# Optimization experiments

Measured on AMD Instinct MI355X. Metric: run time of the kernel, lower is better.

The kernel has to match this reference:

```python
import jax, jax.numpy as jnp
import numpy as np

N = 8192
IN = 32          # Config.network_in_size
G = 16           # Config.global_size
H1 = 32          # layer1 out
H2 = 16          # lstm vertex out
LSTM_HID = H2 + G      # 48
LSTM_IN = H1 * 3 + G   # 112
L3_IN = H2 * 3 + G     # 64
EPS = 1e-12


def _norm_l1(a):
    # F.normalize(a, p=1, dim=-1): divide by max(L1-norm, eps)
    return a / jnp.maximum(jnp.sum(jnp.abs(a), axis=-1, keepdims=True), EPS)


def _leaky(v):
    return jnp.where(v >= 0, v, 0.01 * v)


def setup_inputs() -> dict:
    key = jax.random.key(0)
    ks = jax.random.split(key, 12)
    s = lambda fan: 1.0 / np.sqrt(fan)
    inp = {
        'adj': jax.random.uniform(ks[0], (N, N), dtype=jnp.float32),
        'x': jax.random.normal(ks[1], (N, IN), dtype=jnp.float32),
        'h': jnp.zeros((N, LSTM_HID), jnp.float32),
        'c': jnp.zeros((N, LSTM_HID), jnp.float32),
        # layer1 GraphLinear(32->32, u->16), input 3*32=96
        'W1': jax.random.uniform(ks[2], (H1, IN * 3), jnp.float32, -s(IN * 3), s(IN * 3)),
        'b1': jnp.zeros((H1,), jnp.float32),
        'uW1': jax.random.uniform(ks[3], (G, IN * 3), jnp.float32, -s(IN * 3), s(IN * 3)),
        'ub1': jnp.zeros((G,), jnp.float32),
        # layer2 LSTM(112 -> 48)
        'Wih': jax.random.uniform(ks[4], (4 * LSTM_HID, LSTM_IN), jnp.float32, -s(LSTM_HID), s(LSTM_HID)),
        'Whh': jax.random.uniform(ks[5], (4 * LSTM_HID, LSTM_HID), jnp.float32, -s(LSTM_HID), s(LSTM_HID)),
        'bih': jnp.zeros((4 * LSTM_HID,), jnp.float32),
        'bhh': jnp.zeros((4 * LSTM_HID,), jnp.float32),
        # layer3 GraphLinear(16->3, in_global=16), input 3*16+16=64
        'W3': jax.random.uniform(ks[6], (3, L3_IN), jnp.float32, -s(L3_IN), s(L3_IN)),
        'b3': jnp.zeros((3,), jnp.float32),
    }
    return inp


def _policy_core(adj, x, h, c, W1, b1, uW1, ub1, Wih, Whh, bih, bhh, W3, b3):
    A = _norm_l1(adj)          # row-normalized adjacency
    AT = _norm_l1(adj.T)       # row-normalized transpose

    # --- layer 1: GraphLinear (no global input) ---
    l1 = jnp.concatenate([A @ x, AT @ x, x], axis=-1)             # [N, 96]
    v1 = _leaky(l1 @ W1.T + b1)                                    # [N, 32]
    u1 = _leaky(jnp.mean(l1, axis=-2) @ uW1.T + ub1)               # [16]

    # --- layer 2: GraphLSTM (seq_len=1, batch=N) ---
    l2 = jnp.concatenate([
        jnp.broadcast_to(u1, (v1.shape[0], G)),
        A @ v1, AT @ v1, v1], axis=-1)                             # [N, 112]
    gates = l2 @ Wih.T + bih + h @ Whh.T + bhh                     # [N, 192]
    i, f, g, o = jnp.split(gates, 4, axis=-1)
    c_out = jax.nn.sigmoid(f) * c + jax.nn.sigmoid(i) * jnp.tanh(g)
    h_out = jax.nn.sigmoid(o) * jnp.tanh(c_out)                    # [N, 48]
    v2 = _leaky(h_out[:, :H2])                                     # [N, 16]
    u2 = _leaky(jnp.mean(h_out[:, H2:], axis=-2))                  # [16]

    # --- layer 3: GraphLinear with global input (no activation) ---
    l3 = jnp.concatenate([
        jnp.broadcast_to(u2, (v2.shape[0], G)),
        A @ v2, AT @ v2, v2], axis=-1)                             # [N, 64]
    x3 = l3 @ W3.T + b3                                            # [N, 3]

    logits = 2.0 * jnp.tanh(x3)
    probs = jax.nn.softmax(logits, axis=-1)
    return probs, logits, h_out, c_out


def reference(adj, x, h, c, W1, b1, uW1, ub1, Wih, Whh, bih, bhh, W3, b3):
    probs, logits, h_out, c_out = _policy_core(
        adj, x, h, c, W1, b1, uW1, ub1, Wih, Whh, bih, bhh, W3, b3)
    # multinomial(probs, 1) == categorical over the same logits
    actions = jax.random.categorical(jax.random.key(42), logits, axis=-1)  # [N]
    return (actions.astype(jnp.float32) - 1.0, h_out, c_out)
```

## Files before the change

### kernel.cpp

```cpp
#include <hip/hip_runtime.h>
#include <stdint.h>
#include <math.h>

#define NROW 8192

constexpr size_t W_FP  = 0;
constexpr size_t W_GP  = W_FP  + (size_t)32*NROW*32;
constexpr size_t W_RSP = W_GP  + (size_t)64*NROW*32;
constexpr size_t W_CSP = W_RSP + (size_t)32*NROW;
constexpr size_t W_RS  = W_CSP + (size_t)64*NROW;
constexpr size_t W_CS  = W_RS  + NROW;
constexpr size_t W_V1  = W_CS  + NROW;
constexpr size_t W_V2  = W_V1  + (size_t)NROW*32;
constexpr size_t W_U1  = W_V2  + (size_t)NROW*16;
constexpr size_t W_MLP = W_U1  + 16;
constexpr size_t W_U2P = W_MLP + (size_t)256*96;

typedef float f32x4 __attribute__((ext_vector_type(4)));
typedef short s16x8 __attribute__((ext_vector_type(8)));

__device__ __forceinline__ float leaky(float v) { return v >= 0.f ? v : 0.01f * v; }
__device__ __forceinline__ float sigf(float v) { return 1.f / (1.f + __expf(-v)); }
__device__ __forceinline__ double leakyd(double v) { return v >= 0. ? v : 0.01 * v; }

__device__ __forceinline__ uint32_t bf16rne(float x) {
  uint32_t b = __float_as_uint(x);
  return (b + 0x7FFFu + ((b >> 16) & 1u)) >> 16;
}
__device__ __forceinline__ float bf2f(short s) {
  return __uint_as_float(((uint32_t)(uint16_t)s) << 16);
}
__device__ __forceinline__ uint32_t packHL(float x) {
  const uint32_t hb = bf16rne(x);
  const float hf = __uint_as_float(hb << 16);
  const uint32_t lb = bf16rne(x - hf);
  return hb | (lb << 16);
}
__device__ __forceinline__ void unpack8(const uint32_t u[8], s16x8& h, s16x8& l) {
  #pragma unroll
  for (int j = 0; j < 8; ++j) { h[j] = (short)(u[j] & 0xffffu); l[j] = (short)(u[j] >> 16); }
}

__device__ __forceinline__ void threefry(uint32_t x0, uint32_t x1, uint32_t& o0, uint32_t& o1) {
  const uint32_t ks0 = 0u, ks1 = 42u;
  const uint32_t ks2 = ks0 ^ ks1 ^ 0x1BD11BDAu;
  uint32_t ks[3] = {ks0, ks1, ks2};
  const int R0[4] = {13, 15, 26, 6};
  const int R1[4] = {17, 29, 16, 24};
  x0 += ks[0]; x1 += ks[1];
  #pragma unroll
  for (int g = 0; g < 5; ++g) {
    const int* R = (g & 1) ? R1 : R0;
    #pragma unroll
    for (int i = 0; i < 4; ++i) {
      x0 += x1;
      x1 = (x1 << R[i]) | (x1 >> (32 - R[i]));
      x1 ^= x0;
    }
    x0 += ks[(g + 1) % 3];
    x1 += ks[(g + 2) % 3] + (uint32_t)(g + 1);
  }
  o0 = x0; o1 = x1;
}

template <int C, bool SUMS>
__global__ __launch_bounds__(256) void k_gemm(const float* __restrict__ adj,
                                              const float* __restrict__ X,
                                              float* __restrict__ Fp,
                                              float* __restrict__ Gp,
                                              float* __restrict__ rsP,
                                              float* __restrict__ csP) {
  constexpr int NT = C / 16;
  __shared__ alignas(16) uint32_t aP[32 * 132];
  __shared__ alignas(16) short X2h[C * 136];
  __shared__ alignas(16) short X2l[C * 136];
  __shared__ alignas(16) short XkH[C * 40];
  __shared__ alignas(16) short XkL[C * 40];
  const int t = threadIdx.x;
  const int iz = blockIdx.x;
  const int kz = blockIdx.y;
  const int I0 = iz * 128;
  const int K0 = kz * 256;
  const int lane = t & 63;
  const int wid = t >> 6;
  const int fm = lane & 15;
  const int fg = lane >> 4;

  if constexpr (C == 32) {
    #pragma unroll
    for (int r = 0; r < 4; ++r) {
      const int i = r * 32 + (t >> 3);
      const int c4 = 4 * (t & 7);
      const float4 v = *(const float4*)&X[(size_t)(I0 + i) * 32 + c4];
      const float vv[4] = {v.x, v.y, v.z, v.w};
      #pragma unroll
      for (int j = 0; j < 4; ++j) {
        const uint32_t p = packHL(vv[j]);
        X2h[(c4 + j) * 136 + i] = (short)(p & 0xffffu);
        X2l[(c4 + j) * 136 + i] = (short)(p >> 16);
      }
    }
  } else {
    if (t < 128) {
      #pragma unroll
      for (int r = 0; r < 4; ++r) {
        const int i = r * 32 + (t >> 2);
        const int c4 = 4 * (t & 3);
        const float4 v = *(const float4*)&X[(size_t)(I0 + i) * 16 + c4];
        const float vv[4] = {v.x, v.y, v.z, v.w};
        #pragma unroll
        for (int j = 0; j < 4; ++j) {
          const uint32_t p = packHL(vv[j]);
          X2h[(c4 + j) * 136 + i] = (short)(p & 0xffffu);
          X2l[(c4 + j) * 136 + i] = (short)(p >> 16);
        }
      }
    }
  }

  f32x4 accF[4][NT];
  #pragma unroll
  for (int mt = 0; mt < 4; ++mt)
    #pragma unroll
    for (int nt = 0; nt < NT; ++nt) accF[mt][nt] = (f32x4){0.f, 0.f, 0.f, 0.f};
  float rs[4] = {0.f, 0.f, 0.f, 0.f};

  const int rb = t >> 3;
  const int k4 = 4 * (t & 7);

  for (int ch = 0; ch < 8; ++ch) {
    const int kb = K0 + ch * 32;
    __syncthreads();
    #pragma unroll
    for (int q = 0; q < 4; ++q) {
      const int i = q * 32 + rb;
      const float4 v = *(const float4*)&adj[(size_t)(I0 + i) * NROW + kb + k4];
      const float vv[4] = {v.x, v.y, v.z, v.w};
      #pragma unroll
      for (int j = 0; j < 4; ++j) aP[(k4 + j) * 132 + i] = packHL(vv[j]);
    }
    if constexpr (C == 32) {
      const int k = t >> 3, c4 = 4 * (t & 7);
      const float4 v = *(const float4*)&X[(size_t)(kb + k) * 32 + c4];
      const float vv[4] = {v.x, v.y, v.z, v.w};
      #pragma unroll
      for (int j = 0; j < 4; ++j) {
        const uint32_t p = packHL(vv[j]);
        XkH[(c4 + j) * 40 + k] = (short)(p & 0xffffu);
        XkL[(c4 + j) * 40 + k] = (short)(p >> 16);
      }
    } else {
      if (t < 128) {
        const int k = t >> 2, c4 = 4 * (t & 3);
        const float4 v = *(const float4*)&X[(size_t)(kb + k) * 16 + c4];
        const float vv[4] = {v.x, v.y, v.z, v.w};
        #pragma unroll
        for (int j = 0; j < 4; ++j) {
          const uint32_t p = packHL(vv[j]);
          XkH[(c4 + j) * 40 + k] = (short)(p & 0xffffu);
          XkL[(c4 + j) * 40 + k] = (short)(p >> 16);
        }
      }
    }
    __syncthreads();
    if (wid < 2) {
      s16x8 bh[NT], bl[NT];
      #pragma unroll
      for (int nt = 0; nt < NT; ++nt) {
        bh[nt] = *(const s16x8*)&XkH[(nt * 16 + fm) * 40 + 8 * fg];
        bl[nt] = *(const s16x8*)&XkL[(nt * 16 + fm) * 40 + 8 * fg];
      }
      #pragma unroll
      for (int mt = 0; mt < 4; ++mt) {
        const int rowl = (wid * 4 + mt) * 16 + fm;
        uint32_t u[8];
        #pragma unroll
        for (int j = 0; j < 8; ++j) u[j] = aP[(8 * fg + j) * 132 + rowl];
        s16x8 ah, al;
        unpack8(u, ah, al);
        if (SUMS) {
          #pragma unroll
          for (int j = 0; j < 8; ++j) rs[mt] += fabsf(bf2f(ah[j]) + bf2f(al[j]));
        }
        #pragma unroll
        for (int nt = 0; nt < NT; ++nt) {
          accF[mt][nt] = __builtin_amdgcn_mfma_f32_16x16x32_bf16(ah, bh[nt], accF[mt][nt], 0, 0, 0);
          accF[mt][nt] = __builtin_amdgcn_mfma_f32_16x16x32_bf16(ah, bl[nt], accF[mt][nt], 0, 0, 0);
          accF[mt][nt] = __builtin_amdgcn_mfma_f32_16x16x32_bf16(al, bh[nt], accF[mt][nt], 0, 0, 0);
        }
      }
    } else {
      const int kt = wid - 2;
      f32x4 accT[NT];
      #pragma unroll
      for (int ct = 0; ct < NT; ++ct) accT[ct] = (f32x4){0.f, 0.f, 0.f, 0.f};
      float cs = 0.f;
      #pragma unroll
      for (int iw = 0; iw < 4; ++iw) {
        const uint32_t* ap = &aP[(kt * 16 + fm) * 132 + iw * 32 + 8 * fg];
        const uint4 ua = *(const uint4*)ap;
        const uint4 ub = *(const uint4*)(ap + 4);
        const uint32_t u[8] = {ua.x, ua.y, ua.z, ua.w, ub.x, ub.y, ub.z, ub.w};
        s16x8 ah, al;
        unpack8(u, ah, al);
        if (SUMS) {
          #pragma unroll
          for (int j = 0; j < 8; ++j) cs += fabsf(bf2f(ah[j]) + bf2f(al[j]));
        }
        #pragma unroll
        for (int ct = 0; ct < NT; ++ct) {
          const s16x8 xh = *(const s16x8*)&X2h[(ct * 16 + fm) * 136 + iw * 32 + 8 * fg];
          const s16x8 xl = *(const s16x8*)&X2l[(ct * 16 + fm) * 136 + iw * 32 + 8 * fg];
          accT[ct] = __builtin_amdgcn_mfma_f32_16x16x32_bf16(ah, xh, accT[ct], 0, 0, 0);
          accT[ct] = __builtin_amdgcn_mfma_f32_16x16x32_bf16(ah, xl, accT[ct], 0, 0, 0);
          accT[ct] = __builtin_amdgcn_mfma_f32_16x16x32_bf16(al, xh, accT[ct], 0, 0, 0);
        }
      }
      #pragma unroll
      for (int ct = 0; ct < NT; ++ct)
        #pragma unroll
        for (int r = 0; r < 4; ++r)
          Gp[((size_t)iz * NROW + kb + kt * 16 + 4 * fg + r) * C + ct * 16 + fm] = accT[ct][r];
      if (SUMS) {
        cs += __shfl_xor(cs, 16, 64);
        cs += __shfl_xor(cs, 32, 64);
        if (lane < 16) csP[(size_t)iz * NROW + kb + kt * 16 + lane] = cs;
      }
    }
  }
  if (wid < 2) {
    #pragma unroll
    for (int mt = 0; mt < 4; ++mt) {
      const int rowb = I0 + (wid * 4 + mt) * 16;
      #pragma unroll
      for (int nt = 0; nt < NT; ++nt)
        #pragma unroll
        for (int r = 0; r < 4; ++r)
          Fp[((size_t)kz * NROW + rowb + 4 * fg + r) * C + nt * 16 + fm] = accF[mt][nt][r];
      if (SUMS) {
        float v = rs[mt];
        v += __shfl_xor(v, 16, 64);
        v += __shfl_xor(v, 32, 64);
        if (lane < 16) rsP[(size_t)kz * NROW + rowb + lane] = v;
      }
    }
  }
}

__global__ __launch_bounds__(256) void k_s1(const float* __restrict__ Fp, const float* __restrict__ rsP,
                                            const float* __restrict__ Gp, const float* __restrict__ csP,
                                            const float* __restrict__ x,  const float* __restrict__ W1,
                                            const float* __restrict__ b1,
                                            float* __restrict__ rowsum, float* __restrict__ colsum,
                                            float* __restrict__ v1, float* __restrict__ mlp) {
  __shared__ float l1L[32 * 100];
  __shared__ float rsL[32], csL[32];
  const int t = threadIdx.x;
  const int n0 = blockIdx.x * 32;
  if (t < 32) {
    double s = 0.;
    for (int p = 0; p < 32; ++p) s += (double)rsP[(size_t)p * NROW + n0 + t];
    s = fmax(s, 1e-12);
    rowsum[n0 + t] = (float)s; rsL[t] = (float)s;
  } else if (t < 64) {
    const int r = t - 32;
    double s = 0.;
    for (int p = 0; p < 64; ++p) s += (double)csP[(size_t)p * NROW + n0 + r];
    s = fmax(s, 1e-12);
    colsum[n0 + r] = (float)s; csL[r] = (float)s;
  }
  __syncthreads();
  {
    const int r = t >> 3, c = (t & 7) * 4;
    const int n = n0 + r;
    double s[4] = {0., 0., 0., 0.};
    for (int p = 0; p < 32; ++p) {
      const float4 v = *(const float4*)&Fp[((size_t)p * NROW + n) * 32 + c];
      s[0] += v.x; s[1] += v.y; s[2] += v.z; s[3] += v.w;
    }
    const double rsv = (double)rsL[r];
    #pragma unroll
    for (int q = 0; q < 4; ++q) l1L[r * 100 + c + q] = (float)(s[q] / rsv);
    double sg[4] = {0., 0., 0., 0.};
    for (int p = 0; p < 64; ++p) {
      const float4 v = *(const float4*)&Gp[((size_t)p * NROW + n) * 32 + c];
      sg[0] += v.x; sg[1] += v.y; sg[2] += v.z; sg[3] += v.w;
    }
    const double csv = (double)csL[r];
    #pragma unroll
    for (int q = 0; q < 4; ++q) l1L[r * 100 + 32 + c + q] = (float)(sg[q] / csv);
    *(float4*)&l1L[r * 100 + 64 + c] = *(const float4*)&x[(size_t)n * 32 + c];
  }
  __syncthreads();
  if (t < 96) {
    double s = 0.;
    for (int r = 0; r < 32; ++r) s += (double)l1L[r * 100 + t];
    mlp[(size_t)blockIdx.x * 96 + t] = (float)s;
  }
  {
    const int r = t & 31, jg = t >> 5;
    const int n = n0 + r;
    float accv[4];
    #pragma unroll
    for (int jj = 0; jj < 4; ++jj) accv[jj] = b1[4 * jg + jj];
    for (int k = 0; k < 96; k += 4) {
      const float4 lv = *(const float4*)&l1L[r * 100 + k];
      #pragma unroll
      for (int jj = 0; jj < 4; ++jj) {
        const float4 wv = *(const float4*)&W1[(size_t)(4 * jg + jj) * 96 + k];
        accv[jj] += lv.x * wv.x + lv.y * wv.y + lv.z * wv.z + lv.w * wv.w;
      }
    }
    #pragma unroll
    for (int jj = 0; jj < 4; ++jj) v1[(size_t)n * 32 + 4 * jg + jj] = leaky(accv[jj]);
  }
}

__global__ void k_s2(const float* __restrict__ mlp, const float* __restrict__ uW1,
                     const float* __restrict__ ub1, float* __restrict__ u1) {
  __shared__ float ml[96];
  const int t = threadIdx.x;
  if (t < 96) {
    double s = 0.;
    for (int b = 0; b < 256; ++b) s += (double)mlp[(size_t)b * 96 + t];
    ml[t] = (float)(s * (1.0 / 8192.0));
  }
  __syncthreads();
  if (t < 16) {
    double a = (double)ub1[t];
    for (int k = 0; k < 96; ++k) a += (double)ml[k] * (double)uW1[(size_t)t * 96 + k];
    u1[t] = (float)leakyd(a);
  }
}

__global__ __launch_bounds__(256) void k_s4(const float* __restrict__ Fp, const float* __restrict__ Gp,
                                            const float* __restrict__ v1, const float* __restrict__ u1,
                                            const float* __restrict__ rowsum, const float* __restrict__ colsum,
                                            const float* __restrict__ Wih, const float* __restrict__ Whh,
                                            const float* __restrict__ bih, const float* __restrict__ bhh,
                                            const float* __restrict__ h_in, const float* __restrict__ c_in,
                                            float* __restrict__ out, float* __restrict__ v2,
                                            float* __restrict__ u2p) {
  __shared__ float vecL[16 * 148];
  __shared__ float gL[16 * 132];
  __shared__ float rsL[16], csL[16];
  __shared__ float hoL[16 * 17];
  const int t = threadIdx.x;
  const int n0 = blockIdx.x * 16;
  if (t < 16) rsL[t] = rowsum[n0 + t];
  else if (t < 32) csL[t - 16] = colsum[n0 + t - 16];
  { const int r = t >> 4, k = t & 15; vecL[r * 148 + k] = u1[k]; }
  __syncthreads();
  {
    const int r = t >> 4, q = t & 15;
    const int n = n0 + r;
    if (q < 8) {
      const int c = q * 4;
      float4 s = {0.f, 0.f, 0.f, 0.f};
      for (int p = 0; p < 32; ++p) {
        const float4 v = *(const float4*)&Fp[((size_t)p * NROW + n) * 32 + c];
        s.x += v.x; s.y += v.y; s.z += v.z; s.w += v.w;
      }
      const float rsv = rsL[r];
      float4 o = {s.x / rsv, s.y / rsv, s.z / rsv, s.w / rsv};
      *(float4*)&vecL[r * 148 + 16 + c] = o;
      *(float4*)&vecL[r * 148 + 80 + c] = *(const float4*)&v1[(size_t)n * 32 + c];
    } else {
      const int c = (q - 8) * 4;
      float4 s = {0.f, 0.f, 0.f, 0.f};
      for (int p = 0; p < 64; ++p) {
        const float4 v = *(const float4*)&Gp[((size_t)p * NROW + n) * 32 + c];
        s.x += v.x; s.y += v.y; s.z += v.z; s.w += v.w;
      }
      const float csv = csL[r];
      float4 o = {s.x / csv, s.y / csv, s.z / csv, s.w / csv};
      *(float4*)&vecL[r * 148 + 48 + c] = o;
      *(float4*)&vecL[r * 148 + 112 + c] = *(const float4*)&h_in[(size_t)n * 32 + c];
    }
  }
  __syncthreads();
  {
    const int gate = t & 127;
    const int half = t >> 7;
    const float bias = bih[gate] + bhh[gate];
    float acc[8];
    #pragma unroll
    for (int rr = 0; rr < 8; ++rr) acc[rr] = bias;
    const float* __restrict__ Wrow = Wih + (size_t)gate * 112;
    const float* __restrict__ vbase = vecL + (half * 8) * 148;
    #pragma unroll 4
    for (int kq = 0; kq < 28; ++kq) {
      const float4 w = *(const float4*)&Wrow[kq * 4];
      #pragma unroll
      for (int rr = 0; rr < 8; ++rr) {
        const float4 v = *(const float4*)&vbase[rr * 148 + kq * 4];
        acc[rr] += w.x * v.x + w.y * v.y + w.z * v.z + w.w * v.w;
      }
    }
    const float* __restrict__ Hrow = Whh + (size_t)gate * 32;
    #pragma unroll 4
    for (int kq = 0; kq < 8; ++kq) {
      const float4 w = *(const float4*)&Hrow[kq * 4];
      #pragma unroll
      for (int rr = 0; rr < 8; ++rr) {
        const float4 v = *(const float4*)&vbase[rr * 148 + 112 + kq * 4];
        acc[rr] += w.x * v.x + w.y * v.y + w.z * v.z + w.w * v.w;
      }
    }
    #pragma unroll
    for (int rr = 0; rr < 8; ++rr) gL[(half * 8 + rr) * 132 + gate] = acc[rr];
  }
  __syncthreads();
  #pragma unroll
  for (int it = 0; it < 2; ++it) {
    const int w = it * 256 + t;
    const int r = w >> 5, j = w & 31;
    const int n = n0 + r;
    const float iv = gL[r * 132 + j];
    const float fv = gL[r * 132 + 32 + j];
    const float gv = gL[r * 132 + 64 + j];
    const float ov = gL[r * 132 + 96 + j];
    const float cv = c_in[(size_t)n * 32 + j];
    const float cn = sigf(fv) * cv + sigf(iv) * tanhf(gv);
    const float hn = sigf(ov) * tanhf(cn);
    out[8192 + (size_t)n * 32 + j] = hn;
    out[8192 + 262144 + (size_t)n * 32 + j] = cn;
    if (j < 16) v2[(size_t)n * 16 + j] = leaky(hn);
    else hoL[r * 17 + (j - 16)] = hn;
  }
  __syncthreads();
  if (t < 16) {
    float s = 0.f;
    for (int r2 = 0; r2 < 16; ++r2) s += hoL[r2 * 17 + t];
    u2p[(size_t)blockIdx.x * 16 + t] = s;
  }
}

__global__ __launch_bounds__(256) void k_s6(const float* __restrict__ Fp, const float* __restrict__ Gp,
                                            const float* __restrict__ v2, const float* __restrict__ u2p,
                                            const float* __restrict__ rowsum, const float* __restrict__ colsum,
                                            const float* __restrict__ W3, const float* __restrict__ b3,
                                            float* __restrict__ out) {
  __shared__ float l3L[64 * 68];
  __shared__ float w3L[192];
  __shared__ float b3L[3];
  __shared__ float u2L[16];
  __shared__ double lgL[64 * 4];
  __shared__ float rsL[64], csL[64];
  const int t = threadIdx.x;
  const int n0 = blockIdx.x * 64;
  if (t < 192) w3L[t] = W3[t];
  if (t < 3) b3L[t] = b3[t];
  if (t < 64) rsL[t] = rowsum[n0 + t];
  else if (t < 128) csL[t - 64] = colsum[n0 + t - 64];
  else if (t >= 240) {
    const int j = t - 240;
    double s = 0.;
    for (int b = 0; b < 512; ++b) s += (double)u2p[(size_t)b * 16 + j];
    u2L[j] = (float)leakyd(s * (1.0 / 8192.0));
  }
  __syncthreads();
  {
    const int r = t >> 2, q = t & 3;
    const int n = n0 + r;
    if (q == 0) {
      #pragma unroll
      for (int cc = 0; cc < 4; ++cc) *(float4*)&l3L[r * 68 + cc * 4] = *(const float4*)&u2L[cc * 4];
    } else if (q == 1) {
      const double rsv = (double)rsL[r];
      #pragma unroll
      for (int cc = 0; cc < 4; ++cc) {
        const int c = cc * 4;
        double s[4] = {0., 0., 0., 0.};
        for (int p = 0; p < 32; ++p) {
          const float4 v = *(const float4*)&Fp[((size_t)p * NROW + n) * 16 + c];
          s[0] += v.x; s[1] += v.y; s[2] += v.z; s[3] += v.w;
        }
        #pragma unroll
        for (int q2 = 0; q2 < 4; ++q2) l3L[r * 68 + 16 + c + q2] = (float)(s[q2] / rsv);
      }
    } else if (q == 2) {
      const double csv = (double)csL[r];
      #pragma unroll
      for (int cc = 0; cc < 4; ++cc) {
        const int c = cc * 4;
        double s[4] = {0., 0., 0., 0.};
        for (int p = 0; p < 64; ++p) {
          const float4 v = *(const float4*)&Gp[((size_t)p * NROW + n) * 16 + c];
          s[0] += v.x; s[1] += v.y; s[2] += v.z; s[3] += v.w;
        }
        #pragma unroll
        for (int q2 = 0; q2 < 4; ++q2) l3L[r * 68 + 32 + c + q2] = (float)(s[q2] / csv);
      }
    } else {
      #pragma unroll
      for (int cc = 0; cc < 4; ++cc)
        *(float4*)&l3L[r * 68 + 48 + cc * 4] = *(const float4*)&v2[(size_t)n * 16 + cc * 4];
    }
  }
  __syncthreads();
  {
    const int r = t >> 2, q = t & 3;
    if (q < 3) {
      double a = (double)b3L[q];
      for (int k = 0; k < 64; ++k) a += (double)l3L[r * 68 + k] * (double)w3L[q * 64 + k];
      lgL[r * 4 + q] = 2.0 * tanh(a);
    }
  }
  __syncthreads();
  if ((t & 3) == 0) {
    const int r = t >> 2;
    const int n = n0 + r;
    int best = 0;
    double bv = -1.0e300;
    #pragma unroll
    for (int j = 0; j < 3; ++j) {
      const uint32_t m = (uint32_t)(n * 3 + j);
      uint32_t o0, o1;
      threefry(0u, m, o0, o1);
      const uint32_t bits = o0 ^ o1;
      const float f = __uint_as_float((bits >> 9) | 0x3f800000u) - 1.0f;
      const double u = fmax((double)f, 1.17549435e-38);
      const double g = -log(-log(u));
      const double val = g + lgL[r * 4 + j];
      if (val > bv) { bv = val; best = j; }
    }
    out[n] = (float)best - 1.0f;
  }
}

extern "C" void kernel_launch(void* const* d_in, const int* in_sizes, int n_in,
                              void* d_out, int out_size, void* d_ws, size_t ws_size,
                              hipStream_t stream) {
  const float* adj = (const float*)d_in[0];
  const float* x   = (const float*)d_in[1];
  const float* h   = (const float*)d_in[2];
  const float* c   = (const float*)d_in[3];
  const float* W1  = (const float*)d_in[4];
  const float* b1  = (const float*)d_in[5];
  const float* uW1 = (const float*)d_in[6];
  const float* ub1 = (const float*)d_in[7];
  const float* Wih = (const float*)d_in[8];
  const float* Whh = (const float*)d_in[9];
  const float* bih = (const float*)d_in[10];
  const float* bhh = (const float*)d_in[11];
  const float* W3  = (const float*)d_in[12];
  const float* b3  = (const float*)d_in[13];
  float* out = (float*)d_out;
  float* ws  = (float*)d_ws;

  float* Fp  = ws + W_FP;
  float* Gp  = ws + W_GP;
  float* rsP = ws + W_RSP;
  float* csP = ws + W_CSP;
  float* rs  = ws + W_RS;
  float* cs  = ws + W_CS;
  float* v1  = ws + W_V1;
  float* v2  = ws + W_V2;
  float* u1  = ws + W_U1;
  float* mlp = ws + W_MLP;
  float* u2p = ws + W_U2P;

  k_gemm<32, true><<<dim3(64, 32), 256, 0, stream>>>(adj, x, Fp, Gp, rsP, csP);
  k_s1<<<256, 256, 0, stream>>>(Fp, rsP, Gp, csP, x, W1, b1, rs, cs, v1, mlp);
  k_s2<<<1, 128, 0, stream>>>(mlp, uW1, ub1, u1);

  k_gemm<32, false><<<dim3(64, 32), 256, 0, stream>>>(adj, v1, Fp, Gp, nullptr, nullptr);
  k_s4<<<512, 256, 0, stream>>>(Fp, Gp, v1, u1, rs, cs, Wih, Whh, bih, bhh, h, c, out, v2, u2p);

  k_gemm<16, false><<<dim3(64, 32), 256, 0, stream>>>(adj, v2, Fp, Gp, nullptr, nullptr);
  k_s6<<<128, 256, 0, stream>>>(Fp, Gp, v2, u2p, rs, cs, W3, b3, out);
}
```

Before: 344.3 us.

## Process two row tiles per GEMM block to halve transposed partial-sum slices

Each GEMM block now walks two consecutive 128-row tiles of adj. It keeps the transposed-product accumulators for all eight k-chunks in registers across both tiles and writes them once at the end. This halves the number of Gp and csP partial slices from 64 to 32, which cuts partial-sum write traffic and the reduction loops in the downstream kernels. In exchange it halves the grid to 1024 blocks and adds a large accT register array that could raise register pressure and lower occupancy.

```diff
diff --git a/kernel.cpp b/kernel.cpp
--- a/kernel.cpp
+++ b/kernel.cpp
@@ -6,9 +6,9 @@
 
 constexpr size_t W_FP  = 0;
 constexpr size_t W_GP  = W_FP  + (size_t)32*NROW*32;
-constexpr size_t W_RSP = W_GP  + (size_t)64*NROW*32;
+constexpr size_t W_RSP = W_GP  + (size_t)32*NROW*32;
 constexpr size_t W_CSP = W_RSP + (size_t)32*NROW;
-constexpr size_t W_RS  = W_CSP + (size_t)64*NROW;
+constexpr size_t W_RS  = W_CSP + (size_t)32*NROW;
 constexpr size_t W_CS  = W_RS  + NROW;
 constexpr size_t W_V1  = W_CS  + NROW;
 constexpr size_t W_V2  = W_V1  + (size_t)NROW*32;
@@ -77,36 +77,36 @@
   __shared__ alignas(16) short XkH[C * 40];
   __shared__ alignas(16) short XkL[C * 40];
   const int t = threadIdx.x;
-  const int iz = blockIdx.x;
+  const int bx = blockIdx.x;
   const int kz = blockIdx.y;
-  const int I0 = iz * 128;
   const int K0 = kz * 256;
   const int lane = t & 63;
   const int wid = t >> 6;
   const int fm = lane & 15;
   const int fg = lane >> 4;
-
-  if constexpr (C == 32) {
-    #pragma unroll
-    for (int r = 0; r < 4; ++r) {
-      const int i = r * 32 + (t >> 3);
-      const int c4 = 4 * (t & 7);
-      const float4 v = *(const float4*)&X[(size_t)(I0 + i) * 32 + c4];
-      const float vv[4] = {v.x, v.y, v.z, v.w};
-      #pragma unroll
-      for (int j = 0; j < 4; ++j) {
-        const uint32_t p = packHL(vv[j]);
-        X2h[(c4 + j) * 136 + i] = (short)(p & 0xffffu);
-        X2l[(c4 + j) * 136 + i] = (short)(p >> 16);
-      }
-    }
-  } else {
-    if (t < 128) {
+  const int rb = t >> 3;
+  const int k4 = 4 * (t & 7);
+  const int kt = wid - 2;
+
+  f32x4 accT[8][NT];
+  float csA[8];
+  #pragma unroll
+  for (int ch = 0; ch < 8; ++ch) {
+    csA[ch] = 0.f;
+    #pragma unroll
+    for (int ct = 0; ct < NT; ++ct) accT[ch][ct] = (f32x4){0.f, 0.f, 0.f, 0.f};
+  }
+
+  #pragma unroll
+  for (int half = 0; half < 2; ++half) {
+    const int I0 = (bx * 2 + half) * 128;
+    __syncthreads();
+    if constexpr (C == 32) {
       #pragma unroll
       for (int r = 0; r < 4; ++r) {
-        const int i = r * 32 + (t >> 2);
-        const int c4 = 4 * (t & 3);
-        const float4 v = *(const float4*)&X[(size_t)(I0 + i) * 16 + c4];
+        const int i = r * 32 + (t >> 3);
+        const int c4 = 4 * (t & 7);
+        const float4 v = *(const float4*)&X[(size_t)(I0 + i) * 32 + c4];
         const float vv[4] = {v.x, v.y, v.z, v.w};
         #pragma unroll
         for (int j = 0; j < 4; ++j) {
@@ -115,44 +115,46 @@
           X2l[(c4 + j) * 136 + i] = (short)(p >> 16);
         }
       }
-    }
-  }
-
-  f32x4 accF[4][NT];
-  #pragma unroll
-  for (int mt = 0; mt < 4; ++mt)
-    #pragma unroll
-    for (int nt = 0; nt < NT; ++nt) accF[mt][nt] = (f32x4){0.f, 0.f, 0.f, 0.f};
-  float rs[4] = {0.f, 0.f, 0.f, 0.f};
-
-  const int rb = t >> 3;
-  const int k4 = 4 * (t & 7);
-
-  for (int ch = 0; ch < 8; ++ch) {
-    const int kb = K0 + ch * 32;
-    __syncthreads();
-    #pragma unroll
-    for (int q = 0; q < 4; ++q) {
-      const int i = q * 32 + rb;
-      const float4 v = *(const float4*)&adj[(size_t)(I0 + i) * NROW + kb + k4];
-      const float vv[4] = {v.x, v.y, v.z, v.w};
-      #pragma unroll
-      for (int j = 0; j < 4; ++j) aP[(k4 + j) * 132 + i] = packHL(vv[j]);
-    }
-    if constexpr (C == 32) {
-      const int k = t >> 3, c4 = 4 * (t & 7);
-      const float4 v = *(const float4*)&X[(size_t)(kb + k) * 32 + c4];
-      const float vv[4] = {v.x, v.y, v.z, v.w};
-      #pragma unroll
-      for (int j = 0; j < 4; ++j) {
-        const uint32_t p = packHL(vv[j]);
-        XkH[(c4 + j) * 40 + k] = (short)(p & 0xffffu);
-        XkL[(c4 + j) * 40 + k] = (short)(p >> 16);
-      }
     } else {
       if (t < 128) {
-        const int k = t >> 2, c4 = 4 * (t & 3);
-        const float4 v = *(const float4*)&X[(size_t)(kb + k) * 16 + c4];
+        #pragma unroll
+        for (int r = 0; r < 4; ++r) {
+          const int i = r * 32 + (t >> 2);
+          const int c4 = 4 * (t & 3);
+          const float4 v = *(const float4*)&X[(size_t)(I0 + i) * 16 + c4];
+          const float vv[4] = {v.x, v.y, v.z, v.w};
+          #pragma unroll
+          for (int j = 0; j < 4; ++j) {
+            const uint32_t p = packHL(vv[j]);
+            X2h[(c4 + j) * 136 + i] = (short)(p & 0xffffu);
+            X2l[(c4 + j) * 136 + i] = (short)(p >> 16);
+          }
+        }
+      }
+    }
+
+    f32x4 accF[4][NT];
+    #pragma unroll
+    for (int mt = 0; mt < 4; ++mt)
+      #pragma unroll
+      for (int nt = 0; nt < NT; ++nt) accF[mt][nt] = (f32x4){0.f, 0.f, 0.f, 0.f};
+    float rs[4] = {0.f, 0.f, 0.f, 0.f};
+
+    #pragma unroll
+    for (int ch = 0; ch < 8; ++ch) {
+      const int kb = K0 + ch * 32;
+      __syncthreads();
+      #pragma unroll
+      for (int q = 0; q < 4; ++q) {
+        const int i = q * 32 + rb;
+        const float4 v = *(const float4*)&adj[(size_t)(I0 + i) * NROW + kb + k4];
+        const float vv[4] = {v.x, v.y, v.z, v.w};
+        #pragma unroll
+        for (int j = 0; j < 4; ++j) aP[(k4 + j) * 132 + i] = packHL(vv[j]);
+      }
+      if constexpr (C == 32) {
+        const int k = t >> 3, c4 = 4 * (t & 7);
+        const float4 v = *(const float4*)&X[(size_t)(kb + k) * 32 + c4];
         const float vv[4] = {v.x, v.y, v.z, v.w};
         #pragma unroll
         for (int j = 0; j < 4; ++j) {
@@ -160,88 +162,102 @@
           XkH[(c4 + j) * 40 + k] = (short)(p & 0xffffu);
           XkL[(c4 + j) * 40 + k] = (short)(p >> 16);
         }
-      }
-    }
-    __syncthreads();
+      } else {
+        if (t < 128) {
+          const int k = t >> 2, c4 = 4 * (t & 3);
+          const float4 v = *(const float4*)&X[(size_t)(kb + k) * 16 + c4];
+          const float vv[4] = {v.x, v.y, v.z, v.w};
+          #pragma unroll
+          for (int j = 0; j < 4; ++j) {
+            const uint32_t p = packHL(vv[j]);
+            XkH[(c4 + j) * 40 + k] = (short)(p & 0xffffu);
+            XkL[(c4 + j) * 40 + k] = (short)(p >> 16);
+          }
+        }
+      }
+      __syncthreads();
+      if (wid < 2) {
+        s16x8 bh[NT], bl[NT];
+        #pragma unroll
+        for (int nt = 0; nt < NT; ++nt) {
+          bh[nt] = *(const s16x8*)&XkH[(nt * 16 + fm) * 40 + 8 * fg];
+          bl[nt] = *(const s16x8*)&XkL[(nt * 16 + fm) * 40 + 8 * fg];
+        }
+        #pragma unroll
+        for (int mt = 0; mt < 4; ++mt) {
+          const int rowl = (wid * 4 + mt) * 16 + fm;
+          uint32_t u[8];
+          #pragma unroll
+          for (int j = 0; j < 8; ++j) u[j] = aP[(8 * fg + j) * 132 + rowl];
+          s16x8 ah, al;
+          unpack8(u, ah, al);
+          if (SUMS) {
+            #pragma unroll
+            for (int j = 0; j < 8; ++j) rs[mt] += fabsf(bf2f(ah[j]) + bf2f(al[j]));
+          }
+          #pragma unroll
+          for (int nt = 0; nt < NT; ++nt) {
+            accF[mt][nt] = __builtin_amdgcn_mfma_f32_16x16x32_bf16(ah, bh[nt], accF[mt][nt], 0, 0, 0);
+            accF[mt][nt] = __builtin_amdgcn_mfma_f32_16x16x32_bf16(ah, bl[nt], accF[mt][nt], 0, 0, 0);
+            accF[mt][nt] = __builtin_amdgcn_mfma_f32_16x16x32_bf16(al, bh[nt], accF[mt][nt], 0, 0, 0);
+          }
+        }
+      } else {
+        #pragma unroll
+        for (int iw = 0; iw < 4; ++iw) {
+          const uint32_t* ap = &aP[(kt * 16 + fm) * 132 + iw * 32 + 8 * fg];
+          const uint4 ua = *(const uint4*)ap;
+          const uint4 ub = *(const uint4*)(ap + 4);
+          const uint32_t u[8] = {ua.x, ua.y, ua.z, ua.w, ub.x, ub.y, ub.z, ub.w};
+          s16x8 ah, al;
+          unpack8(u, ah, al);
+          if (SUMS) {
+            #pragma unroll
+            for (int j = 0; j < 8; ++j) csA[ch] += fabsf(bf2f(ah[j]) + bf2f(al[j]));
+          }
+          #pragma unroll
+          for (int ct = 0; ct < NT; ++ct) {
+            const s16x8 xh = *(const s16x8*)&X2h[(ct * 16 + fm) * 136 + iw * 32 + 8 * fg];
+            const s16x8 xl = *(const s16x8*)&X2l[(ct * 16 + fm) * 136 + iw * 32 + 8 * fg];
+            accT[ch][ct] = __builtin_amdgcn_mfma_f32_16x16x32_bf16(ah, xh, accT[ch][ct], 0, 0, 0);
+            accT[ch][ct] = __builtin_amdgcn_mfma_f32_16x16x32_bf16(ah, xl, accT[ch][ct], 0, 0, 0);
+            accT[ch][ct] = __builtin_amdgcn_mfma_f32_16x16x32_bf16(al, xh, accT[ch][ct], 0, 0, 0);
+          }
+        }
+      }
+    }
     if (wid < 2) {
-      s16x8 bh[NT], bl[NT];
-      #pragma unroll
-      for (int nt = 0; nt < NT; ++nt) {
-        bh[nt] = *(const s16x8*)&XkH[(nt * 16 + fm) * 40 + 8 * fg];
-        bl[nt] = *(const s16x8*)&XkL[(nt * 16 + fm) * 40 + 8 * fg];
-      }
       #pragma unroll
       for (int mt = 0; mt < 4; ++mt) {
-        const int rowl = (wid * 4 + mt) * 16 + fm;
-        uint32_t u[8];
-        #pragma unroll
-        for (int j = 0; j < 8; ++j) u[j] = aP[(8 * fg + j) * 132 + rowl];
-        s16x8 ah, al;
-        unpack8(u, ah, al);
+        const int rowb = I0 + (wid * 4 + mt) * 16;
+        #pragma unroll
+        for (int nt = 0; nt < NT; ++nt)
+          #pragma unroll
+          for (int r = 0; r < 4; ++r)
+            Fp[((size_t)kz * NROW + rowb + 4 * fg + r) * C + nt * 16 + fm] = accF[mt][nt][r];
         if (SUMS) {
-          #pragma unroll
-          for (int j = 0; j < 8; ++j) rs[mt] += fabsf(bf2f(ah[j]) + bf2f(al[j]));
-        }
-        #pragma unroll
-        for (int nt = 0; nt < NT; ++nt) {
-          accF[mt][nt] = __builtin_amdgcn_mfma_f32_16x16x32_bf16(ah, bh[nt], accF[mt][nt], 0, 0, 0);
-          accF[mt][nt] = __builtin_amdgcn_mfma_f32_16x16x32_bf16(ah, bl[nt], accF[mt][nt], 0, 0, 0);
-          accF[mt][nt] = __builtin_amdgcn_mfma_f32_16x16x32_bf16(al, bh[nt], accF[mt][nt], 0, 0, 0);
-        }
-      }
-    } else {
-      const int kt = wid - 2;
-      f32x4 accT[NT];
-      #pragma unroll
-      for (int ct = 0; ct < NT; ++ct) accT[ct] = (f32x4){0.f, 0.f, 0.f, 0.f};
-      float cs = 0.f;
-      #pragma unroll
-      for (int iw = 0; iw < 4; ++iw) {
-        const uint32_t* ap = &aP[(kt * 16 + fm) * 132 + iw * 32 + 8 * fg];
-        const uint4 ua = *(const uint4*)ap;
-        const uint4 ub = *(const uint4*)(ap + 4);
-        const uint32_t u[8] = {ua.x, ua.y, ua.z, ua.w, ub.x, ub.y, ub.z, ub.w};
-        s16x8 ah, al;
-        unpack8(u, ah, al);
-        if (SUMS) {
-          #pragma unroll
-          for (int j = 0; j < 8; ++j) cs += fabsf(bf2f(ah[j]) + bf2f(al[j]));
-        }
-        #pragma unroll
-        for (int ct = 0; ct < NT; ++ct) {
-          const s16x8 xh = *(const s16x8*)&X2h[(ct * 16 + fm) * 136 + iw * 32 + 8 * fg];
-          const s16x8 xl = *(const s16x8*)&X2l[(ct * 16 + fm) * 136 + iw * 32 + 8 * fg];
-          accT[ct] = __builtin_amdgcn_mfma_f32_16x16x32_bf16(ah, xh, accT[ct], 0, 0, 0);
-          accT[ct] = __builtin_amdgcn_mfma_f32_16x16x32_bf16(ah, xl, accT[ct], 0, 0, 0);
-          accT[ct] = __builtin_amdgcn_mfma_f32_16x16x32_bf16(al, xh, accT[ct], 0, 0, 0);
-        }
-      }
+          float v = rs[mt];
+          v += __shfl_xor(v, 16, 64);
+          v += __shfl_xor(v, 32, 64);
+          if (lane < 16) rsP[(size_t)kz * NROW + rowb + lane] = v;
+        }
+      }
+    }
+  }
+  if (wid >= 2) {
+    #pragma unroll
+    for (int ch = 0; ch < 8; ++ch) {
+      const int kb = K0 + ch * 32;
       #pragma unroll
       for (int ct = 0; ct < NT; ++ct)
         #pragma unroll
         for (int r = 0; r < 4; ++r)
-          Gp[((size_t)iz * NROW + kb + kt * 16 + 4 * fg + r) * C + ct * 16 + fm] = accT[ct][r];
+          Gp[((size_t)bx * NROW + kb + kt * 16 + 4 * fg + r) * C + ct * 16 + fm] = accT[ch][ct][r];
       if (SUMS) {
+        float cs = csA[ch];
         cs += __shfl_xor(cs, 16, 64);
         cs += __shfl_xor(cs, 32, 64);
-        if (lane < 16) csP[(size_t)iz * NROW + kb + kt * 16 + lane] = cs;
-      }
-    }
-  }
-  if (wid < 2) {
-    #pragma unroll
-    for (int mt = 0; mt < 4; ++mt) {
-      const int rowb = I0 + (wid * 4 + mt) * 16;
-      #pragma unroll
-      for (int nt = 0; nt < NT; ++nt)
-        #pragma unroll
-        for (int r = 0; r < 4; ++r)
-          Fp[((size_t)kz * NROW + rowb + 4 * fg + r) * C + nt * 16 + fm] = accF[mt][nt][r];
-      if (SUMS) {
-        float v = rs[mt];
-        v += __shfl_xor(v, 16, 64);
-        v += __shfl_xor(v, 32, 64);
-        if (lane < 16) rsP[(size_t)kz * NROW + rowb + lane] = v;
+        if (lane < 16) csP[(size_t)bx * NROW + kb + kt * 16 + lane] = cs;
       }
     }
   }
@@ -265,7 +281,7 @@
   } else if (t < 64) {
     const int r = t - 32;
     double s = 0.;
-    for (int p = 0; p < 64; ++p) s += (double)csP[(size_t)p * NROW + n0 + r];
+    for (int p = 0; p < 32; ++p) s += (double)csP[(size_t)p * NROW + n0 + r];
     s = fmax(s, 1e-12);
     colsum[n0 + r] = (float)s; csL[r] = (float)s;
   }
@@ -282,7 +298,7 @@
     #pragma unroll
     for (int q = 0; q < 4; ++q) l1L[r * 100 + c + q] = (float)(s[q] / rsv);
     double sg[4] = {0., 0., 0., 0.};
-    for (int p = 0; p < 64; ++p) {
+    for (int p = 0; p < 32; ++p) {
       const float4 v = *(const float4*)&Gp[((size_t)p * NROW + n) * 32 + c];
       sg[0] += v.x; sg[1] += v.y; sg[2] += v.z; sg[3] += v.w;
     }
@@ -368,7 +384,7 @@
     } else {
       const int c = (q - 8) * 4;
       float4 s = {0.f, 0.f, 0.f, 0.f};
-      for (int p = 0; p < 64; ++p) {
+      for (int p = 0; p < 32; ++p) {
         const float4 v = *(const float4*)&Gp[((size_t)p * NROW + n) * 32 + c];
         s.x += v.x; s.y += v.y; s.z += v.z; s.w += v.w;
       }
@@ -485,7 +501,7 @@
       for (int cc = 0; cc < 4; ++cc) {
         const int c = cc * 4;
         double s[4] = {0., 0., 0., 0.};
-        for (int p = 0; p < 64; ++p) {
+        for (int p = 0; p < 32; ++p) {
           const float4 v = *(const float4*)&Gp[((size_t)p * NROW + n) * 16 + c];
           s[0] += v.x; s[1] += v.y; s[2] += v.z; s[3] += v.w;
         }
@@ -561,13 +577,13 @@
   float* mlp = ws + W_MLP;
   float* u2p = ws + W_U2P;
 
-  k_gemm<32, true><<<dim3(64, 32), 256, 0, stream>>>(adj, x, Fp, Gp, rsP, csP);
+  k_gemm<32, true><<<dim3(32, 32), 256, 0, stream>>>(adj, x, Fp, Gp, rsP, csP);
   k_s1<<<256, 256, 0, stream>>>(Fp, rsP, Gp, csP, x, W1, b1, rs, cs, v1, mlp);
   k_s2<<<1, 128, 0, stream>>>(mlp, uW1, ub1, u1);
 
-  k_gemm<32, false><<<dim3(64, 32), 256, 0, stream>>>(adj, v1, Fp, Gp, nullptr, nullptr);
+  k_gemm<32, false><<<dim3(32, 32), 256, 0, stream>>>(adj, v1, Fp, Gp, nullptr, nullptr);
   k_s4<<<512, 256, 0, stream>>>(Fp, Gp, v1, u1, rs, cs, Wih, Whh, bih, bhh, h, c, out, v2, u2p);
 
-  k_gemm<16, false><<<dim3(64, 32), 256, 0, stream>>>(adj, v2, Fp, Gp, nullptr, nullptr);
+  k_gemm<16, false><<<dim3(32, 32), 256, 0, stream>>>(adj, v2, Fp, Gp, nullptr, nullptr);
   k_s6<<<128, 256, 0, stream>>>(Fp, Gp, v2, u2p, rs, cs, W3, b3, out);
 }
```

Result: slower. 479.8 us (+39.4%).
